# Optimization experiments

Hardware: AMD Instinct MI355X
Metric: run time of the kernel (lower is better)

Reference implementation:

```python
import jax, jax.numpy as jnp
import numpy as np

N_ATOMS = 65536
N_SPECIES = 4
N_MOL = 512
F_PS = 512
F_MP = 256
H = 256
EPS = 1e-5


def _layer_norm(x, gamma, beta):
    mu = jnp.mean(x, axis=-1, keepdims=True)
    var = jnp.mean(jnp.square(x - mu), axis=-1, keepdims=True)
    return (x - mu) * jax.lax.rsqrt(var + EPS) * gamma + beta


def _species_mlp(x, W1, W2, W3):
    # x: [N, F], atoms grouped into S contiguous equal-size species blocks.
    S = W1.shape[0]
    N, F = x.shape
    xs = x.reshape(S, N // S, F)                       # [S, N/S, F]
    h = jax.nn.silu(jnp.einsum('snf,sfh->snh', xs, W1))  # grouped GEMM + SiLU
    h = jax.nn.silu(jnp.einsum('snh,sho->sno', h, W2))
    e = jnp.einsum('snh,sho->sno', h, W3)              # [S, N/S, 1]
    return e.reshape(N, -1)                            # keys_to_samples: back to per-atom


def setup_inputs() -> dict:
    key = jax.random.key(0)
    ks = jax.random.split(key, 10)
    inp = {
        'x_ps': jax.random.normal(ks[0], (N_ATOMS, F_PS), dtype=jnp.float32),
        'x_mp': jax.random.normal(ks[1], (N_ATOMS, F_MP), dtype=jnp.float32),
        'batch': jax.random.randint(ks[2], (N_ATOMS,), 0, N_MOL),
        'gamma_ps': jnp.ones((F_PS,), jnp.float32),
        'beta_ps': jnp.zeros((F_PS,), jnp.float32),
        'gamma_mp': jnp.ones((F_MP,), jnp.float32),
        'beta_mp': jnp.zeros((F_MP,), jnp.float32),
        'W_ps1': jax.random.normal(ks[3], (N_SPECIES, F_PS, H), jnp.float32) / np.sqrt(F_PS),
        'W_ps2': jax.random.normal(ks[4], (N_SPECIES, H, H), jnp.float32) / np.sqrt(H),
        'W_ps3': jax.random.normal(ks[5], (N_SPECIES, H, 1), jnp.float32) / np.sqrt(H),
        'W_mp1': jax.random.normal(ks[6], (N_SPECIES, F_MP, H), jnp.float32) / np.sqrt(F_MP),
        'W_mp2': jax.random.normal(ks[7], (N_SPECIES, H, H), jnp.float32) / np.sqrt(H),
        'W_mp3': jax.random.normal(ks[8], (N_SPECIES, H, 1), jnp.float32) / np.sqrt(H),
    }
    return inp


def reference(x_ps, x_mp, batch, gamma_ps, beta_ps, gamma_mp, beta_mp,
              W_ps1, W_ps2, W_ps3, W_mp1, W_mp2, W_mp3):
    norm_factor = jnp.float32(1.0)  # normalization_factor buffer
    f_ps = _layer_norm(x_ps, gamma_ps, beta_ps)
    f_mp = _layer_norm(x_mp, gamma_mp, beta_mp)
    e_ps = _species_mlp(f_ps, W_ps1, W_ps2, W_ps3)   # [N, 1] per-atom energies
    e_mp = _species_mlp(f_mp, W_mp1, W_mp2, W_mp3)   # [N, 1]
    # index_add_ scatter: per-atom -> per-molecule
    energies_ps = jax.ops.segment_sum(e_ps, batch, num_segments=N_MOL) / norm_factor
    energies_mp = jax.ops.segment_sum(e_mp, batch, num_segments=N_MOL) / norm_factor
    return energies_ps + energies_mp                 # [N_MOL, 1] (training path)
```

## Files before the change

kernel.cpp:

```cpp
#include <hip/hip_runtime.h>

#define N_ATOMS 65536
#define N_MOL 512

typedef __attribute__((ext_vector_type(8))) __bf16 bf16x8;
typedef __attribute__((ext_vector_type(4))) float f32x4;

__device__ __forceinline__ unsigned int f2bf(float f) {
    unsigned int u = __float_as_uint(f);
    return (u + 0x7fffu + ((u >> 16) & 1u)) >> 16;
}

__device__ __forceinline__ int pack2(float a, float b) {
    return (int)(f2bf(a) | (f2bf(b) << 16));
}

__device__ __forceinline__ float silu(float v) {
    return v / (1.0f + __expf(-v));
}

#define GLDS16(gp, lp)                                                        \
    __builtin_amdgcn_global_load_lds(                                         \
        (__attribute__((address_space(1))) void*)(uintptr_t)(gp),             \
        (__attribute__((address_space(3))) void*)(uintptr_t)(lp), 16, 0, 0)

#define WS_W1PS 0
#define WS_W2PS 524288
#define WS_W1MP 786432
#define WS_W2MP 1048576
#define WS_GB_BYTES 2621440

__global__ __launch_bounds__(256) void prep_w(const float* __restrict__ Wps1,
                                              const float* __restrict__ Wps2,
                                              const float* __restrict__ Wmp1,
                                              const float* __restrict__ Wmp2,
                                              const float* __restrict__ g_ps,
                                              const float* __restrict__ b_ps,
                                              const float* __restrict__ g_mp,
                                              const float* __restrict__ b_mp,
                                              short* __restrict__ wdst,
                                              float* __restrict__ gb) {
    __shared__ short Ts[16384];
    int b = blockIdx.x;
    const float* src; int K; long dstbase; int s, c;
    const float* ga = nullptr; const float* be = nullptr; float* gbd = nullptr;
    if (b < 32)      { src = Wps1; K = 512; s = b >> 3;        c = b & 7;        dstbase = WS_W1PS;
                       ga = g_ps; be = b_ps; gbd = gb; }
    else if (b < 48) { src = Wps2; K = 256; s = (b - 32) >> 2; c = (b - 32) & 3; dstbase = WS_W2PS; }
    else if (b < 64) { src = Wmp1; K = 256; s = (b - 48) >> 2; c = (b - 48) & 3; dstbase = WS_W1MP;
                       ga = g_mp; be = b_mp; gbd = gb + 2048; }
    else             { src = Wmp2; K = 256; s = (b - 64) >> 2; c = (b - 64) & 3; dstbase = WS_W2MP; }
    int n = threadIdx.x;
    int k0 = c * 64;
    const float* sp = src + (long)s * K * 256 + (long)k0 * 256 + n;
    if (ga) {
        float gs = 0.0f, bs = 0.0f;
        #pragma unroll 4
        for (int kl = 0; kl < 64; ++kl) {
            float v = sp[(long)kl * 256];
            unsigned int h = f2bf(v * ga[k0 + kl]);
            gs += __uint_as_float(h << 16);
            bs += be[k0 + kl] * v;
            int klc = kl & 31, ch = kl >> 5;
            int i16 = n * 4 + ((klc >> 3) ^ ((n >> 1) & 3));
            Ts[ch * 8192 + i16 * 8 + (klc & 7)] = (short)h;
        }
        atomicAdd(&gbd[s * 256 + n], gs);
        atomicAdd(&gbd[1024 + s * 256 + n], bs);
    } else {
        #pragma unroll 4
        for (int kl = 0; kl < 64; ++kl) {
            unsigned int h = f2bf(sp[(long)kl * 256]);
            int klc = kl & 31, ch = kl >> 5;
            int i16 = n * 4 + ((klc >> 3) ^ ((n >> 1) & 3));
            Ts[ch * 8192 + i16 * 8 + (klc & 7)] = (short)h;
        }
    }
    __syncthreads();
    long base = dstbase + (long)s * K * 256 + (long)c * 16384;
    int4* dp = (int4*)(wdst + base);
    const int4* tp = (const int4*)Ts;
    #pragma unroll
    for (int i = 0; i < 8; ++i) dp[threadIdx.x + i * 256] = tp[threadIdx.x + i * 256];
}

__global__ __launch_bounds__(256, 3) void mlp_all(
    const float* __restrict__ x_ps, const float* __restrict__ x_mp,
    const short* __restrict__ wimg, const float* __restrict__ gb,
    const float* __restrict__ W3ps, const float* __restrict__ W3mp,
    const int* __restrict__ batch, float* __restrict__ out) {
    __shared__ short As[2048];
    __shared__ short Bs[8192];
    __shared__ short H1[16384];
    __shared__ float2 rowstats[64];
    __shared__ float e_lds[64];

    const int tid = threadIdx.x;
    const int lane = tid & 63;
    const int wid = tid >> 6;
    const int wn = wid * 64;
    const int lg = lane >> 4;
    const int ln = lane & 15;

    const bool mp = blockIdx.x >= 1024;
    const int tile = mp ? (int)blockIdx.x - 1024 : (int)blockIdx.x;
    const float* x = mp ? x_mp : x_ps;
    const int F = mp ? 256 : 512;
    const int nch1 = F >> 5;
    const int block0 = tile * 64;
    const int species = block0 >> 14;
    const short* W1 = wimg + (mp ? WS_W1MP : WS_W1PS) + (size_t)species * F * 256;
    const short* W2 = wimg + (mp ? WS_W2MP : WS_W2PS) + (size_t)species * 65536;
    const float* gW1 = gb + (mp ? 2048 : 0) + species * 256;
    const float* bW1 = gW1 + 1024;
    const float* W3 = (mp ? W3mp : W3ps) + species * 256;

    if (tid < 64) e_lds[tid] = 0.0f;

    const int ar = tid >> 2;
    const int aj = tid & 3;
    const float* xrow = x + (size_t)(block0 + ar) * F + aj * 8;

    f32x4 acc[4][4];
    #pragma unroll
    for (int m = 0; m < 4; ++m)
        #pragma unroll
        for (int n = 0; n < 4; ++n) acc[m][n] = (f32x4){0.f, 0.f, 0.f, 0.f};
    float s1 = 0.0f, s2 = 0.0f;

    for (int c = 0; c < nch1; ++c) {
        if (c) __syncthreads();
        {
            const int4* gsrc = (const int4*)(W1 + (size_t)c * 8192);
            int4* bsl = (int4*)Bs;
            #pragma unroll
            for (int q = 0; q < 4; ++q) {
                int idx = wid * 256 + q * 64;
                GLDS16(gsrc + idx + lane, bsl + idx);
            }
        }
        {
            const float4 u = *(const float4*)(xrow + c * 32);
            const float4 v = *(const float4*)(xrow + c * 32 + 4);
            s1 += u.x + u.y + u.z + u.w + v.x + v.y + v.z + v.w;
            s2 += u.x * u.x + u.y * u.y + u.z * u.z + u.w * u.w
                + v.x * v.x + v.y * v.y + v.z * v.z + v.w * v.w;
            int4 p;
            p.x = pack2(u.x, u.y); p.y = pack2(u.z, u.w);
            p.z = pack2(v.x, v.y); p.w = pack2(v.z, v.w);
            int i16 = ar * 4 + (aj ^ ((ar >> 1) & 3));
            *(int4*)&As[i16 * 8] = p;
        }
        __syncthreads();
        bf16x8 a[4], b[4];
        #pragma unroll
        for (int m = 0; m < 4; ++m) {
            int row = m * 16 + ln;
            int i16 = row * 4 + (lg ^ ((row >> 1) & 3));
            a[m] = *(const bf16x8*)&As[i16 * 8];
        }
        #pragma unroll
        for (int n = 0; n < 4; ++n) {
            int col = wn + n * 16 + ln;
            int i16 = col * 4 + (lg ^ ((col >> 1) & 3));
            b[n] = *(const bf16x8*)&Bs[i16 * 8];
        }
        #pragma unroll
        for (int m = 0; m < 4; ++m)
            #pragma unroll
            for (int n = 0; n < 4; ++n)
                acc[m][n] = __builtin_amdgcn_mfma_f32_16x16x32_bf16(a[m], b[n], acc[m][n], 0, 0, 0);
    }

    s1 += __shfl_xor(s1, 1); s1 += __shfl_xor(s1, 2);
    s2 += __shfl_xor(s2, 1); s2 += __shfl_xor(s2, 2);
    if (aj == 0) rowstats[ar] = make_float2(s1, s2);
    __syncthreads();

    float gwv[4], bwv[4], w3v[4];
    #pragma unroll
    for (int n = 0; n < 4; ++n) {
        int col = wn + n * 16 + ln;
        gwv[n] = gW1[col]; bwv[n] = bW1[col]; w3v[n] = W3[col];
    }
    const float invF = mp ? (1.0f / 256.0f) : (1.0f / 512.0f);
    #pragma unroll
    for (int m = 0; m < 4; ++m) {
        #pragma unroll
        for (int rr = 0; rr < 4; ++rr) {
            int row = m * 16 + lg * 4 + rr;
            float2 rs = rowstats[row];
            float mu = rs.x * invF;
            float var = rs.y * invF - mu * mu;
            float rstd = rsqrtf(var + 1e-5f);
            float nmu = rstd * mu;
            #pragma unroll
            for (int n = 0; n < 4; ++n) {
                float v = rstd * acc[m][n][rr] - nmu * gwv[n] + bwv[n];
                int col = wn + n * 16 + ln;
                H1[(row * 256 + col) ^ ((row & 7) << 3)] = (short)f2bf(silu(v));
            }
        }
    }

    f32x4 acc2[4][4];
    #pragma unroll
    for (int m = 0; m < 4; ++m)
        #pragma unroll
        for (int n = 0; n < 4; ++n) acc2[m][n] = (f32x4){0.f, 0.f, 0.f, 0.f};

    for (int c = 0; c < 8; ++c) {
        __syncthreads();
        {
            const int4* gsrc = (const int4*)(W2 + (size_t)c * 8192);
            int4* bsl = (int4*)Bs;
            #pragma unroll
            for (int q = 0; q < 4; ++q) {
                int idx = wid * 256 + q * 64;
                GLDS16(gsrc + idx + lane, bsl + idx);
            }
        }
        __syncthreads();
        bf16x8 a[4], b[4];
        #pragma unroll
        for (int m = 0; m < 4; ++m) {
            int row = m * 16 + ln;
            int e = (row * 256 + c * 32 + lg * 8) ^ ((row & 7) << 3);
            a[m] = *(const bf16x8*)&H1[e];
        }
        #pragma unroll
        for (int n = 0; n < 4; ++n) {
            int col = wn + n * 16 + ln;
            int i16 = col * 4 + (lg ^ ((col >> 1) & 3));
            b[n] = *(const bf16x8*)&Bs[i16 * 8];
        }
        #pragma unroll
        for (int m = 0; m < 4; ++m)
            #pragma unroll
            for (int n = 0; n < 4; ++n)
                acc2[m][n] = __builtin_amdgcn_mfma_f32_16x16x32_bf16(a[m], b[n], acc2[m][n], 0, 0, 0);
    }

    #pragma unroll
    for (int m = 0; m < 4; ++m) {
        #pragma unroll
        for (int rr = 0; rr < 4; ++rr) {
            int row = m * 16 + lg * 4 + rr;
            float p = 0.0f;
            #pragma unroll
            for (int n = 0; n < 4; ++n) p += silu(acc2[m][n][rr]) * w3v[n];
            p += __shfl_xor(p, 1); p += __shfl_xor(p, 2);
            p += __shfl_xor(p, 4); p += __shfl_xor(p, 8);
            if (ln == 0) atomicAdd(&e_lds[row], p);
        }
    }
    __syncthreads();
    if (tid < 64) atomicAdd(out + batch[block0 + tid], e_lds[tid]);
}

extern "C" void kernel_launch(void* const* d_in, const int* in_sizes, int n_in,
                              void* d_out, int out_size, void* d_ws, size_t ws_size,
                              hipStream_t stream) {
    const float* x_ps     = (const float*)d_in[0];
    const float* x_mp     = (const float*)d_in[1];
    const int*   batch    = (const int*)d_in[2];
    const float* gamma_ps = (const float*)d_in[3];
    const float* beta_ps  = (const float*)d_in[4];
    const float* gamma_mp = (const float*)d_in[5];
    const float* beta_mp  = (const float*)d_in[6];
    const float* W_ps1    = (const float*)d_in[7];
    const float* W_ps2    = (const float*)d_in[8];
    const float* W_ps3    = (const float*)d_in[9];
    const float* W_mp1    = (const float*)d_in[10];
    const float* W_mp2    = (const float*)d_in[11];
    const float* W_mp3    = (const float*)d_in[12];

    float* out = (float*)d_out;
    short* wsW = (short*)d_ws;
    float* gb  = (float*)((char*)d_ws + WS_GB_BYTES);

    hipMemsetAsync(out, 0, N_MOL * sizeof(float), stream);
    hipMemsetAsync(gb, 0, 4096 * sizeof(float), stream);

    hipLaunchKernelGGL(prep_w, dim3(80), dim3(256), 0, stream,
                       W_ps1, W_ps2, W_mp1, W_mp2,
                       gamma_ps, beta_ps, gamma_mp, beta_mp, wsW, gb);

    hipLaunchKernelGGL(mlp_all, dim3(2048), dim3(256), 0, stream,
                       x_ps, x_mp, wsW, gb, W_ps3, W_mp3, batch, out);
}
```

Before: 147.6 us.

## Double-buffer W1/activation tiles and prefetch across GEMM stages in fused MLP

Restructures the fused two-layer MLP kernel into a templated body, specialized per feature width so the chunk loops can be fully unrolled. The first GEMM now uses double-buffered LDS for weights and activations, with activation registers prefetched two chunks ahead and the next weight chunk issued via async global-to-LDS loads before the MFMAs. The first W2 chunk is prefetched during the last W1 chunk, and the batch indices and per-column parameters are loaded early. This aims to hide global load latency behind compute, at the cost of a larger shared-memory arena that aliases H1 onto the second B buffer and the A buffers, plus more register pressure.

```diff
diff --git a/kernel.cpp b/kernel.cpp
--- a/kernel.cpp
+++ b/kernel.cpp
@@ -84,16 +84,29 @@
     for (int i = 0; i < 8; ++i) dp[threadIdx.x + i * 256] = tp[threadIdx.x + i * 256];
 }
 
-__global__ __launch_bounds__(256, 3) void mlp_all(
-    const float* __restrict__ x_ps, const float* __restrict__ x_mp,
-    const short* __restrict__ wimg, const float* __restrict__ gb,
-    const float* __restrict__ W3ps, const float* __restrict__ W3mp,
-    const int* __restrict__ batch, float* __restrict__ out) {
-    __shared__ short As[2048];
-    __shared__ short Bs[8192];
-    __shared__ short H1[16384];
-    __shared__ float2 rowstats[64];
-    __shared__ float e_lds[64];
+#define OFF_BS0   0
+#define OFF_BS1   16384
+#define OFF_AS0   32768
+#define OFF_AS1   36864
+#define OFF_H1    16384
+#define OFF_STATS 49152
+#define OFF_ELDS  49664
+#define ARENA_BYTES 49920
+
+template <int NCH>
+__device__ __forceinline__ void mlp_body(
+    char* arena,
+    const float* __restrict__ x, const short* __restrict__ W1,
+    const short* __restrict__ W2, const float* __restrict__ gW1,
+    const float* __restrict__ bW1, const float* __restrict__ W3,
+    const int* __restrict__ batch, float* __restrict__ out, int tile) {
+    short* Bs0 = (short*)(arena + OFF_BS0);
+    short* Bs1 = (short*)(arena + OFF_BS1);
+    short* As0 = (short*)(arena + OFF_AS0);
+    short* As1 = (short*)(arena + OFF_AS1);
+    short* H1  = (short*)(arena + OFF_H1);
+    float2* rowstats = (float2*)(arena + OFF_STATS);
+    float*  e_lds    = (float*)(arena + OFF_ELDS);
 
     const int tid = threadIdx.x;
     const int lane = tid & 63;
@@ -101,25 +114,29 @@
     const int wn = wid * 64;
     const int lg = lane >> 4;
     const int ln = lane & 15;
-
-    const bool mp = blockIdx.x >= 1024;
-    const int tile = mp ? (int)blockIdx.x - 1024 : (int)blockIdx.x;
-    const float* x = mp ? x_mp : x_ps;
-    const int F = mp ? 256 : 512;
-    const int nch1 = F >> 5;
+    const int swz = lg ^ ((ln >> 1) & 3);
+
     const int block0 = tile * 64;
     const int species = block0 >> 14;
-    const short* W1 = wimg + (mp ? WS_W1MP : WS_W1PS) + (size_t)species * F * 256;
-    const short* W2 = wimg + (mp ? WS_W2MP : WS_W2PS) + (size_t)species * 65536;
-    const float* gW1 = gb + (mp ? 2048 : 0) + species * 256;
-    const float* bW1 = gW1 + 1024;
-    const float* W3 = (mp ? W3mp : W3ps) + species * 256;
+    const short* W1s = W1 + (size_t)species * NCH * 8192;
+    const short* W2s = W2 + (size_t)species * 65536;
 
     if (tid < 64) e_lds[tid] = 0.0f;
+    int mol = (tid < 64) ? batch[block0 + tid] : 0;
+
+    float gwv[4], bwv[4], w3v[4];
+    #pragma unroll
+    for (int n = 0; n < 4; ++n) {
+        int col = wn + n * 16 + ln;
+        gwv[n] = gW1[species * 256 + col];
+        bwv[n] = bW1[species * 256 + col];
+        w3v[n] = W3[species * 256 + col];
+    }
 
     const int ar = tid >> 2;
     const int aj = tid & 3;
-    const float* xrow = x + (size_t)(block0 + ar) * F + aj * 8;
+    const float* xrow = x + (size_t)(block0 + ar) * (NCH * 32) + aj * 8;
+    const int i16a = ar * 4 + (aj ^ ((ar >> 1) & 3));
 
     f32x4 acc[4][4];
     #pragma unroll
@@ -128,42 +145,62 @@
         for (int n = 0; n < 4; ++n) acc[m][n] = (f32x4){0.f, 0.f, 0.f, 0.f};
     float s1 = 0.0f, s2 = 0.0f;
 
-    for (int c = 0; c < nch1; ++c) {
-        if (c) __syncthreads();
-        {
-            const int4* gsrc = (const int4*)(W1 + (size_t)c * 8192);
-            int4* bsl = (int4*)Bs;
+    float4 xu0 = *(const float4*)(xrow);
+    float4 xv0 = *(const float4*)(xrow + 4);
+    float4 xu1 = *(const float4*)(xrow + 32);
+    float4 xv1 = *(const float4*)(xrow + 36);
+    {
+        const int4* gsrc = (const int4*)W1s;
+        int4* bsl = (int4*)Bs0;
+        #pragma unroll
+        for (int q = 0; q < 4; ++q) {
+            int idx = wid * 256 + q * 64;
+            GLDS16(gsrc + idx + lane, bsl + idx);
+        }
+    }
+
+    #pragma unroll
+    for (int c = 0; c < NCH; ++c) {
+        const int buf = c & 1;
+        float4 u = buf ? xu1 : xu0;
+        float4 v = buf ? xv1 : xv0;
+        s1 += u.x + u.y + u.z + u.w + v.x + v.y + v.z + v.w;
+        s2 += u.x * u.x + u.y * u.y + u.z * u.z + u.w * u.w
+            + v.x * v.x + v.y * v.y + v.z * v.z + v.w * v.w;
+        int4 p;
+        p.x = pack2(u.x, u.y); p.y = pack2(u.z, u.w);
+        p.z = pack2(v.x, v.y); p.w = pack2(v.z, v.w);
+        *(int4*)&(buf ? As1 : As0)[i16a * 8] = p;
+        __syncthreads();
+        if (c + 2 < NCH) {
+            if (buf) { xu1 = *(const float4*)(xrow + (c + 2) * 32); xv1 = *(const float4*)(xrow + (c + 2) * 32 + 4); }
+            else     { xu0 = *(const float4*)(xrow + (c + 2) * 32); xv0 = *(const float4*)(xrow + (c + 2) * 32 + 4); }
+        }
+        const short* Asr = buf ? As1 : As0;
+        const short* Bsr = buf ? Bs1 : Bs0;
+        bf16x8 a[4], b[4];
+        #pragma unroll
+        for (int m = 0; m < 4; ++m)
+            a[m] = *(const bf16x8*)&Asr[(m * 64 + ln * 4 + swz) * 8];
+        #pragma unroll
+        for (int n = 0; n < 4; ++n)
+            b[n] = *(const bf16x8*)&Bsr[(wn * 4 + n * 64 + ln * 4 + swz) * 8];
+        if (c + 1 < NCH) {
+            const int4* gsrc = (const int4*)(W1s + (size_t)(c + 1) * 8192);
+            int4* bsl = (int4*)(buf ? Bs0 : Bs1);
             #pragma unroll
             for (int q = 0; q < 4; ++q) {
                 int idx = wid * 256 + q * 64;
                 GLDS16(gsrc + idx + lane, bsl + idx);
             }
-        }
-        {
-            const float4 u = *(const float4*)(xrow + c * 32);
-            const float4 v = *(const float4*)(xrow + c * 32 + 4);
-            s1 += u.x + u.y + u.z + u.w + v.x + v.y + v.z + v.w;
-            s2 += u.x * u.x + u.y * u.y + u.z * u.z + u.w * u.w
-                + v.x * v.x + v.y * v.y + v.z * v.z + v.w * v.w;
-            int4 p;
-            p.x = pack2(u.x, u.y); p.y = pack2(u.z, u.w);
-            p.z = pack2(v.x, v.y); p.w = pack2(v.z, v.w);
-            int i16 = ar * 4 + (aj ^ ((ar >> 1) & 3));
-            *(int4*)&As[i16 * 8] = p;
-        }
-        __syncthreads();
-        bf16x8 a[4], b[4];
-        #pragma unroll
-        for (int m = 0; m < 4; ++m) {
-            int row = m * 16 + ln;
-            int i16 = row * 4 + (lg ^ ((row >> 1) & 3));
-            a[m] = *(const bf16x8*)&As[i16 * 8];
-        }
-        #pragma unroll
-        for (int n = 0; n < 4; ++n) {
-            int col = wn + n * 16 + ln;
-            int i16 = col * 4 + (lg ^ ((col >> 1) & 3));
-            b[n] = *(const bf16x8*)&Bs[i16 * 8];
+        } else {
+            const int4* gsrc = (const int4*)W2s;
+            int4* bsl = (int4*)Bs0;
+            #pragma unroll
+            for (int q = 0; q < 4; ++q) {
+                int idx = wid * 256 + q * 64;
+                GLDS16(gsrc + idx + lane, bsl + idx);
+            }
         }
         #pragma unroll
         for (int m = 0; m < 4; ++m)
@@ -177,13 +214,7 @@
     if (aj == 0) rowstats[ar] = make_float2(s1, s2);
     __syncthreads();
 
-    float gwv[4], bwv[4], w3v[4];
-    #pragma unroll
-    for (int n = 0; n < 4; ++n) {
-        int col = wn + n * 16 + ln;
-        gwv[n] = gW1[col]; bwv[n] = bW1[col]; w3v[n] = W3[col];
-    }
-    const float invF = mp ? (1.0f / 256.0f) : (1.0f / 512.0f);
+    const float invF = 1.0f / (float)(NCH * 32);
     #pragma unroll
     for (int m = 0; m < 4; ++m) {
         #pragma unroll
@@ -196,9 +227,9 @@
             float nmu = rstd * mu;
             #pragma unroll
             for (int n = 0; n < 4; ++n) {
-                float v = rstd * acc[m][n][rr] - nmu * gwv[n] + bwv[n];
+                float vv = rstd * acc[m][n][rr] - nmu * gwv[n] + bwv[n];
                 int col = wn + n * 16 + ln;
-                H1[(row * 256 + col) ^ ((row & 7) << 3)] = (short)f2bf(silu(v));
+                H1[(row * 256 + col) ^ ((row & 7) << 3)] = (short)f2bf(silu(vv));
             }
         }
     }
@@ -209,31 +240,26 @@
         #pragma unroll
         for (int n = 0; n < 4; ++n) acc2[m][n] = (f32x4){0.f, 0.f, 0.f, 0.f};
 
+    #pragma unroll
     for (int c = 0; c < 8; ++c) {
         __syncthreads();
-        {
-            const int4* gsrc = (const int4*)(W2 + (size_t)c * 8192);
-            int4* bsl = (int4*)Bs;
+        bf16x8 a[4], b[4];
+        #pragma unroll
+        for (int m = 0; m < 4; ++m)
+            a[m] = *(const bf16x8*)&H1[m * 4096 + ln * 256 + ((c * 32 + lg * 8) ^ ((ln & 7) << 3))];
+        #pragma unroll
+        for (int n = 0; n < 4; ++n)
+            b[n] = *(const bf16x8*)&Bs0[(wn * 4 + n * 64 + ln * 4 + swz) * 8];
+        __syncthreads();
+        if (c < 7) {
+            const int4* gsrc = (const int4*)(W2s + (size_t)(c + 1) * 8192);
+            int4* bsl = (int4*)Bs0;
             #pragma unroll
             for (int q = 0; q < 4; ++q) {
                 int idx = wid * 256 + q * 64;
                 GLDS16(gsrc + idx + lane, bsl + idx);
             }
         }
-        __syncthreads();
-        bf16x8 a[4], b[4];
-        #pragma unroll
-        for (int m = 0; m < 4; ++m) {
-            int row = m * 16 + ln;
-            int e = (row * 256 + c * 32 + lg * 8) ^ ((row & 7) << 3);
-            a[m] = *(const bf16x8*)&H1[e];
-        }
-        #pragma unroll
-        for (int n = 0; n < 4; ++n) {
-            int col = wn + n * 16 + ln;
-            int i16 = col * 4 + (lg ^ ((col >> 1) & 3));
-            b[n] = *(const bf16x8*)&Bs[i16 * 8];
-        }
         #pragma unroll
         for (int m = 0; m < 4; ++m)
             #pragma unroll
@@ -255,7 +281,22 @@
         }
     }
     __syncthreads();
-    if (tid < 64) atomicAdd(out + batch[block0 + tid], e_lds[tid]);
+    if (tid < 64) atomicAdd(out + mol, e_lds[tid]);
+}
+
+__global__ __launch_bounds__(256, 3) void mlp_all(
+    const float* __restrict__ x_ps, const float* __restrict__ x_mp,
+    const short* __restrict__ wimg, const float* __restrict__ gb,
+    const float* __restrict__ W3ps, const float* __restrict__ W3mp,
+    const int* __restrict__ batch, float* __restrict__ out) {
+    __shared__ __align__(16) char arena[ARENA_BYTES];
+    if (blockIdx.x < 1024) {
+        mlp_body<16>(arena, x_ps, wimg + WS_W1PS, wimg + WS_W2PS,
+                     gb + 0, gb + 1024, W3ps, batch, out, (int)blockIdx.x);
+    } else {
+        mlp_body<8>(arena, x_mp, wimg + WS_W1MP, wimg + WS_W2MP,
+                    gb + 2048, gb + 3072, W3mp, batch, out, (int)blockIdx.x - 1024);
+    }
 }
 
 extern "C" void kernel_launch(void* const* d_in, const int* in_sizes, int n_in,
```

After: 200.5 us. 35.9% more time.
